# Performance work log

Measured on AMD Instinct MI355X. Metric: run time of the kernel, lower is better.

## Reference

```python
import jax, jax.numpy as jnp
import numpy as np

C_IN, CH, HCH, NFFT, HOP, NL, K = 100, 512, 1536, 1024, 256, 8, 4
B, T = 16, 1024

def conv1d(x, w, b=None, pad=0, groups=1):
    # x: [B, Cin, L], w: [Cout, Cin/groups, K]
    y = jax.lax.conv_general_dilated(x, w, (1,), [(pad, pad)],
        dimension_numbers=('NCH', 'OIH', 'NCH'), feature_group_count=groups)
    if b is not None:
        y = y + b[None, :, None]
    return y

def layernorm(x, g, b, eps=1e-5):
    # normalize over last axis (channel), torch LayerNorm semantics (biased var)
    mu = jnp.mean(x, -1, keepdims=True)
    var = jnp.var(x, -1, keepdims=True)
    return (x - mu) * jax.lax.rsqrt(var + eps) * g + b

def setup_inputs() -> dict:
    key = jax.random.key(0)
    ks = jax.random.split(key, 8)
    r = lambda k, s: jax.random.normal(k, s, jnp.float32) * 0.02
    return {
        'x': jax.random.normal(ks[0], (B, C_IN, T), jnp.float32),
        'in_w': r(ks[1], (CH, C_IN, 7)), 'in_b': jnp.zeros((CH,), jnp.float32),
        'norm_g': jnp.ones((CH,), jnp.float32), 'norm_b': jnp.zeros((CH,), jnp.float32),
        'dw_w': r(ks[2], (NL, CH, 1, 7)), 'dw_b': jnp.zeros((NL, CH), jnp.float32),
        'ln_g': jnp.ones((NL, CH), jnp.float32), 'ln_b': jnp.zeros((NL, CH), jnp.float32),
        'pw1_w': r(ks[3], (NL, HCH, CH)), 'pw1_b': jnp.zeros((NL, HCH), jnp.float32),
        'pw2_w': r(ks[4], (NL, CH, HCH)), 'pw2_b': jnp.zeros((NL, CH), jnp.float32),
        'ls': jnp.full((NL, CH), 1.0 / NL, jnp.float32),
        'normL_g': jnp.ones((CH,), jnp.float32), 'normL_b': jnp.zeros((CH,), jnp.float32),
        'out_w': r(ks[5], (NFFT, CH, 1)), 'out_b': jnp.zeros((NFFT,), jnp.float32),
        'ov_w': r(ks[6], (HOP, NFFT, K)),
    }

def reference(x, in_w, in_b, norm_g, norm_b, dw_w, dw_b, ln_g, ln_b,
              pw1_w, pw1_b, pw2_w, pw2_b, ls, normL_g, normL_b, out_w, out_b, ov_w):
    x = conv1d(x, in_w, in_b, pad=3)                                   # [B, CH, T]
    x = layernorm(x.transpose(0, 2, 1), norm_g, norm_b).transpose(0, 2, 1)

    def layer(h, p):
        dw, db, g, b, w1, b1, w2, b2, s = p
        y = conv1d(h, dw, db, pad=3, groups=CH)                        # depthwise 7-tap
        y = layernorm(y.transpose(0, 2, 1), g, b)                      # [B, T, CH]
        y = jnp.einsum('btc,hc->bth', y, w1) + b1                      # pointwise expand
        y = jax.nn.gelu(y, approximate=False)
        y = jnp.einsum('bth,ch->btc', y, w2) + b2                      # pointwise project
        return h + (y * s).transpose(0, 2, 1), None

    x, _ = jax.lax.scan(layer, x, (dw_w, dw_b, ln_g, ln_b, pw1_w, pw1_b, pw2_w, pw2_b, ls))
    x = layernorm(x.transpose(0, 2, 1), normL_g, normL_b).transpose(0, 2, 1)
    o = conv1d(x, out_w, out_b, pad=0)                                 # [B, NFFT, T]
    # --- overlap_add ---
    o = conv1d(o, ov_w, None, pad=K - 1)                               # [B, HOP, L], L = T + K - 1
    Bn, C, L = o.shape
    pad_size = C * K - L + K - 1
    o = jnp.pad(o, ((0, 0), (0, 0), (0, pad_size)))
    idx = (jnp.arange(L)[None, :] + jnp.arange(C)[:, None] * (C * K - 1)) % L  # [C, L]
    o = jnp.take_along_axis(o, jnp.broadcast_to(idx[None], (Bn, C, L)), axis=2)
    o = jnp.sum(o, axis=1, keepdims=True)                              # [B, 1, L]
    return o[..., K // 2 : L - K // 2 + 1]                             # [B, 1, T]
```

## Files before the change

kernel.cpp:

```cpp
#include <hip/hip_runtime.h>

#define B_    16
#define CIN   100
#define T_    1024
#define CH_   512
#define HCH_  1536
#define NL_   8
#define NFFT_ 1024
#define HOP_  256
#define BT    (B_ * T_)
#define L_    1027
#define OROWS 1032
#define KIN   704

typedef __bf16 bf16x8 __attribute__((ext_vector_type(8)));
typedef float f32x4 __attribute__((ext_vector_type(4)));
typedef short s16x8 __attribute__((ext_vector_type(8)));

__device__ __forceinline__ short f2b(float f) {
  unsigned u = __float_as_uint(f);
  u += 0x7fffu + ((u >> 16) & 1u);
  return (short)(u >> 16);
}
__device__ __forceinline__ float b2f(short s) {
  return __uint_as_float(((unsigned)(unsigned short)s) << 16);
}

__device__ __forceinline__ void gl2lds16(const void* g, void* l) {
  __builtin_amdgcn_global_load_lds(
      (__attribute__((address_space(1))) void*)g,
      (__attribute__((address_space(3))) void*)l, 16, 0, 0);
}

__global__ __launch_bounds__(256) void k_cvt(const float* __restrict__ s,
                                             short* __restrict__ d, int n) {
  for (int i = blockIdx.x * 256 + threadIdx.x; i < n; i += gridDim.x * 256)
    d[i] = f2b(s[i]);
}

__global__ __launch_bounds__(256) void k_cvt_ov(const float* __restrict__ w,
                                                short* __restrict__ d) {
  const int n = 4 * HOP_ * NFFT_;
  for (int i = blockIdx.x * 256 + threadIdx.x; i < n; i += gridDim.x * 256) {
    int k = i >> 18;
    int rem = i & 0x3FFFF;
    int c = rem >> 10, nn = rem & 1023;
    d[i] = f2b(w[((size_t)c * NFFT_ + nn) * 4 + k]);
  }
}

__global__ __launch_bounds__(256) void k_cvt_inw(const float* __restrict__ w,
                                                 short* __restrict__ d) {
  const int n = CH_ * KIN;
  for (int i = blockIdx.x * 256 + threadIdx.x; i < n; i += gridDim.x * 256) {
    int c = i / KIN, e = i - c * KIN;
    d[i] = (e < 700) ? f2b(w[c * 700 + e]) : (short)0;
  }
}

__global__ __launch_bounds__(256) void k_cvt_dwt(const float* __restrict__ w,
                                                 float* __restrict__ d) {
  const int n = NL_ * 7 * CH_;
  for (int i = blockIdx.x * 256 + threadIdx.x; i < n; i += gridDim.x * 256) {
    int l = i / (7 * CH_), r = i - l * 7 * CH_;
    int k = r >> 9, c = r & 511;
    d[i] = w[((size_t)l * CH_ + c) * 7 + k];
  }
}

__global__ __launch_bounds__(256) void k_im2col(const float* __restrict__ x,
                                                short* __restrict__ xim) {
  const int total = BT * KIN;
  for (int i = blockIdx.x * 256 + threadIdx.x; i < total; i += gridDim.x * 256) {
    int m = i / KIN, e = i - m * KIN;
    int b = m >> 10, t = m & 1023;
    int ci = e / 7, k = e - ci * 7;
    int tt = t + k - 3;
    float v = (e < 700 && tt >= 0 && tt < T_) ? x[((b * CIN + ci) << 10) + tt] : 0.f;
    xim[i] = f2b(v);
  }
}

__global__ __launch_bounds__(256) void k_zeropad(short* __restrict__ o1p) {
  int i = blockIdx.x * 256 + threadIdx.x;
  int b = i >> 13;
  int r8 = (i >> 10) & 7;
  int nn = i & 1023;
  int row = r8 < 4 ? r8 : (OROWS - 8 + r8);
  o1p[((size_t)b * OROWS + row) * NFFT_ + nn] = 0;
}

__global__ __launch_bounds__(256) void k_lnb(const short* __restrict__ in,
                                             short* __restrict__ outp,
                                             const float* __restrict__ g,
                                             const float* __restrict__ bta) {
  int row = blockIdx.x, tid = threadIdx.x;
  unsigned u = *reinterpret_cast<const unsigned*>(&in[(size_t)row * CH_ + tid * 2]);
  float v0 = __uint_as_float(u << 16);
  float v1 = __uint_as_float(u & 0xffff0000u);
  float s = v0 + v1, q = v0 * v0 + v1 * v1;
#pragma unroll
  for (int o = 32; o > 0; o >>= 1) { s += __shfl_down(s, o); q += __shfl_down(q, o); }
  __shared__ float sh[8];
  int wid = tid >> 6, lane = tid & 63;
  if (lane == 0) { sh[wid] = s; sh[wid + 4] = q; }
  __syncthreads();
  float S = sh[0] + sh[1] + sh[2] + sh[3];
  float Q = sh[4] + sh[5] + sh[6] + sh[7];
  float mu  = S * (1.f / 512.f);
  float var = Q * (1.f / 512.f) - mu * mu;
  float r = rsqrtf(var + 1e-5f);
  float x0 = (v0 - mu) * r * g[tid * 2]     + bta[tid * 2];
  float x1 = (v1 - mu) * r * g[tid * 2 + 1] + bta[tid * 2 + 1];
  unsigned o = ((unsigned)(unsigned short)f2b(x0)) |
               (((unsigned)(unsigned short)f2b(x1)) << 16);
  *reinterpret_cast<unsigned*>(&outp[(size_t)row * CH_ + tid * 2]) = o;
}

__global__ __launch_bounds__(256) void k_dwln(const short* __restrict__ h,
                                              const float* __restrict__ dwt,
                                              const float* __restrict__ dwb,
                                              const float* __restrict__ g,
                                              const float* __restrict__ bta,
                                              short* __restrict__ yb) {
  int b = blockIdx.x, t0 = blockIdx.y * 32;
  int tid = threadIdx.x, lane = tid & 63, w = tid >> 6;
  __shared__ short hs[38][512];
  for (int e = tid; e < 38 * 64; e += 256) {
    int row = e >> 6, seg = (e & 63) << 3;
    int t = t0 - 3 + row;
    s16x8 v = {};
    if (t >= 0 && t < T_)
      v = *reinterpret_cast<const s16x8*>(&h[((size_t)((b << 10) + t)) * CH_ + seg]);
    *reinterpret_cast<s16x8*>(&hs[row][seg]) = v;
  }
  const int c0 = lane << 3;
  float wk[7][8];
#pragma unroll
  for (int k = 0; k < 7; ++k) {
    f32x4 lo = *reinterpret_cast<const f32x4*>(&dwt[k * CH_ + c0]);
    f32x4 hi = *reinterpret_cast<const f32x4*>(&dwt[k * CH_ + c0 + 4]);
#pragma unroll
    for (int j = 0; j < 4; ++j) { wk[k][j] = lo[j]; wk[k][j + 4] = hi[j]; }
  }
  float bb[8], gg[8], be[8];
  {
    f32x4 a = *reinterpret_cast<const f32x4*>(&dwb[c0]);
    f32x4 b4 = *reinterpret_cast<const f32x4*>(&dwb[c0 + 4]);
    f32x4 c = *reinterpret_cast<const f32x4*>(&g[c0]);
    f32x4 d = *reinterpret_cast<const f32x4*>(&g[c0 + 4]);
    f32x4 e = *reinterpret_cast<const f32x4*>(&bta[c0]);
    f32x4 f = *reinterpret_cast<const f32x4*>(&bta[c0 + 4]);
#pragma unroll
    for (int j = 0; j < 4; ++j) {
      bb[j] = a[j]; bb[j + 4] = b4[j];
      gg[j] = c[j]; gg[j + 4] = d[j];
      be[j] = e[j]; be[j + 4] = f[j];
    }
  }
  __syncthreads();
#pragma unroll
  for (int i = 0; i < 8; ++i) {
    int r = w * 8 + i;
    float acc[8];
#pragma unroll
    for (int j = 0; j < 8; ++j) acc[j] = bb[j];
#pragma unroll
    for (int k = 0; k < 7; ++k) {
      s16x8 hv = *reinterpret_cast<const s16x8*>(&hs[r + k][c0]);
#pragma unroll
      for (int j = 0; j < 8; ++j) acc[j] += b2f(hv[j]) * wk[k][j];
    }
    float s = 0.f, q = 0.f;
#pragma unroll
    for (int j = 0; j < 8; ++j) { s += acc[j]; q += acc[j] * acc[j]; }
#pragma unroll
    for (int o = 32; o > 0; o >>= 1) { s += __shfl_xor(s, o); q += __shfl_xor(q, o); }
    float mu  = s * (1.f / 512.f);
    float var = q * (1.f / 512.f) - mu * mu;
    float rr = rsqrtf(var + 1e-5f);
    s16x8 ov;
#pragma unroll
    for (int j = 0; j < 8; ++j) ov[j] = f2b((acc[j] - mu) * rr * gg[j] + be[j]);
    *reinterpret_cast<s16x8*>(&yb[((size_t)((b << 10) + t0 + r)) * CH_ + c0]) = ov;
  }
}

template <int MODE>
__global__ __launch_bounds__(256) void k_mgemm(const short* __restrict__ A,
                                               const short* __restrict__ Bw,
                                               const float* __restrict__ bias,
                                               const float* __restrict__ scale,
                                               short* __restrict__ obf,
                                               int N, int K) {
  __shared__ __align__(16) short smem[2 * 128 * 64];
  short* As = smem;
  short* Bs = smem + 128 * 64;
  const int tid = threadIdx.x;
  const int lane = tid & 63, w = tid >> 6;
  const int id = blockIdx.x;
  const int ny = N >> 7;
  const int g8 = id >> 3;
  const int gq = g8 / ny;
  const int mt = (id & 7) + (gq << 3);
  const int nt = g8 - gq * ny;
  const int m0 = mt << 7, n0 = nt << 7;
  const int wr = (w >> 1) * 64, wc = (w & 1) * 64;
  f32x4 acc[4][4];
#pragma unroll
  for (int i = 0; i < 4; ++i)
#pragma unroll
    for (int j = 0; j < 4; ++j) acc[i][j] = (f32x4){0.f, 0.f, 0.f, 0.f};

  const short* Ab = A + (size_t)m0 * K;
  const short* Bb = Bw + (size_t)n0 * K;
  int r_[4], kk_[4];
#pragma unroll
  for (int j = 0; j < 4; ++j) {
    int c = tid + j * 256;
    r_[j] = c >> 3;
    kk_[j] = (((c & 7) ^ (r_[j] & 7)) * 8);
  }
  short* AsB[4]; short* BsB[4];
#pragma unroll
  for (int j = 0; j < 4; ++j) {
    AsB[j] = As + (j * 256 + w * 64) * 8;
    BsB[j] = Bs + (j * 256 + w * 64) * 8;
  }
  const int ar = wr + (lane & 15);
  const int br = wc + (lane & 15);
  const int hi = lane >> 4;

  for (int k0 = 0; k0 < K; k0 += 64) {
#pragma unroll
    for (int j = 0; j < 4; ++j) gl2lds16(Ab + (size_t)r_[j] * K + k0 + kk_[j], AsB[j]);
#pragma unroll
    for (int j = 0; j < 4; ++j) gl2lds16(Bb + (size_t)r_[j] * K + k0 + kk_[j], BsB[j]);
    asm volatile("s_waitcnt vmcnt(0)" ::: "memory");
    __syncthreads();
#pragma unroll
    for (int ks = 0; ks < 2; ++ks) {
      bf16x8 a[4], b[4];
#pragma unroll
      for (int f = 0; f < 4; ++f) {
        int row = ar + f * 16;
        a[f] = *reinterpret_cast<const bf16x8*>(&As[row * 64 + (((ks * 4 + hi) ^ (row & 7)) * 8)]);
      }
#pragma unroll
      for (int f = 0; f < 4; ++f) {
        int row = br + f * 16;
        b[f] = *reinterpret_cast<const bf16x8*>(&Bs[row * 64 + (((ks * 4 + hi) ^ (row & 7)) * 8)]);
      }
#pragma unroll
      for (int fi = 0; fi < 4; ++fi)
#pragma unroll
        for (int fj = 0; fj < 4; ++fj)
          acc[fi][fj] = __builtin_amdgcn_mfma_f32_16x16x32_bf16(a[fi], b[fj], acc[fi][fj], 0, 0, 0);
    }
    __syncthreads();
  }
  short* Cl = smem;
  const int colbase = wc + (lane & 15);
#pragma unroll
  for (int fj = 0; fj < 4; ++fj) {
    int cl = colbase + fj * 16;
    int n = n0 + cl;
    float bi = bias[n];
    float sc = (MODE == 2) ? scale[n] : 0.f;
#pragma unroll
    for (int fi = 0; fi < 4; ++fi) {
#pragma unroll
      for (int r = 0; r < 4; ++r) {
        int rl = wr + (hi << 2) + fi * 16 + r;
        float v = acc[fi][fj][r] + bi;
        if (MODE == 1) v = 0.5f * v * (1.f + erff(v * 0.70710678118654752440f));
        if (MODE == 2) v *= sc;
        Cl[rl * 128 + (cl ^ (((rl >> 2) & 3) << 4))] = f2b(v);
      }
    }
  }
  __syncthreads();
  const int cs = (lane & 15) * 8;
#pragma unroll
  for (int it = 0; it < 8; ++it) {
    int rl = w * 32 + it * 4 + (lane >> 4);
    s16x8 v = *reinterpret_cast<const s16x8*>(&Cl[rl * 128 + (cs ^ (((rl >> 2) & 3) << 4))]);
    int m = m0 + rl;
    if (MODE == 2) {
      size_t idx = (size_t)m * N + n0 + cs;
      s16x8 hv = *reinterpret_cast<const s16x8*>(&obf[idx]);
      s16x8 o;
#pragma unroll
      for (int j = 0; j < 8; ++j) o[j] = f2b(b2f(hv[j]) + b2f(v[j]));
      *reinterpret_cast<s16x8*>(&obf[idx]) = o;
    } else if (MODE == 3) {
      int bb = m >> 10, t = m & 1023;
      *reinterpret_cast<s16x8*>(&obf[((size_t)(bb * OROWS + 4 + t)) * NFFT_ + n0 + cs]) = v;
    } else {
      *reinterpret_cast<s16x8*>(&obf[(size_t)m * N + n0 + cs]) = v;
    }
  }
}

__global__ __launch_bounds__(256) void k_ovgemm(const short* __restrict__ o1p,
                                                const short* __restrict__ ovb,
                                                float* __restrict__ o2) {
  __shared__ __align__(16) short As[136 * 64];
  __shared__ __align__(16) short Bs[128 * 64];
  const int tid = threadIdx.x;
  const int lane = tid & 63, w = tid >> 6;
  const int l0 = blockIdx.x * 128, c0 = blockIdx.y * 128, b = blockIdx.z;
  const int wr = (w >> 1) * 64, wc = (w & 1) * 64;
  f32x4 acc[4][4];
#pragma unroll
  for (int i = 0; i < 4; ++i)
#pragma unroll
    for (int j = 0; j < 4; ++j) acc[i][j] = (f32x4){0.f, 0.f, 0.f, 0.f};

  const short* Ab = o1p + (size_t)b * OROWS * NFFT_;
  const int ar = wr + (lane & 15);
  const int br = wc + (lane & 15);
  const int hi = lane >> 4;
  const int sl_row = lane >> 3;
  const int sl_j   = lane & 7;

  for (int k0 = 0; k0 < NFFT_; k0 += 64) {
    for (int c = w; c < 17; c += 4) {
      int lr = c * 8 + sl_row;
      int gr = l0 + 1 + lr;
      if (gr > OROWS - 1) gr = OROWS - 1;
      int j = sl_j ^ (lr & 7);
      gl2lds16(Ab + (size_t)gr * NFFT_ + k0 + j * 8, As + c * 512);
    }
#pragma unroll
    for (int ksh = 0; ksh < 4; ++ksh) {
      const short* Bb = ovb + ((size_t)(ksh * HOP_ + c0)) * NFFT_;
#pragma unroll
      for (int c = 0; c < 4; ++c) {
        int ch = w * 4 + c;
        int lr = ch * 8 + sl_row;
        int j = sl_j ^ (lr & 7);
        gl2lds16(Bb + (size_t)lr * NFFT_ + k0 + j * 8, Bs + ch * 512);
      }
      asm volatile("s_waitcnt vmcnt(0)" ::: "memory");
      __syncthreads();
#pragma unroll
      for (int ks = 0; ks < 2; ++ks) {
        bf16x8 a[4], bfr[4];
#pragma unroll
        for (int f = 0; f < 4; ++f) {
          int row = ar + f * 16 + ksh;
          a[f] = *reinterpret_cast<const bf16x8*>(&As[row * 64 + (((ks * 4 + hi) ^ (row & 7)) * 8)]);
        }
#pragma unroll
        for (int f = 0; f < 4; ++f) {
          int row = br + f * 16;
          bfr[f] = *reinterpret_cast<const bf16x8*>(&Bs[row * 64 + (((ks * 4 + hi) ^ (row & 7)) * 8)]);
        }
#pragma unroll
        for (int fi = 0; fi < 4; ++fi)
#pragma unroll
          for (int fj = 0; fj < 4; ++fj)
            acc[fi][fj] = __builtin_amdgcn_mfma_f32_16x16x32_bf16(a[fi], bfr[fj], acc[fi][fj], 0, 0, 0);
      }
      __syncthreads();
    }
  }
  const int lb = l0 + wr + (hi << 2);
  const int cb = c0 + wc + (lane & 15);
#pragma unroll
  for (int fj = 0; fj < 4; ++fj) {
    int c = cb + fj * 16;
#pragma unroll
    for (int fi = 0; fi < 4; ++fi) {
#pragma unroll
      for (int r = 0; r < 4; ++r) {
        int l = lb + fi * 16 + r;
        if (l < L_) o2[((size_t)b * L_ + l) * HOP_ + c] = acc[fi][fj][r];
      }
    }
  }
}

__global__ __launch_bounds__(256) void k_oadd(const float* __restrict__ o2,
                                              float* __restrict__ out) {
  int b = blockIdx.x;
  int t = blockIdx.y * 256 + threadIdx.x;
  int m = t + 2;
  float s = 0.f;
  for (int c = 0; c < HOP_; ++c) {
    s += o2[((size_t)b * L_ + m) * HOP_ + c];
    m -= 4;
    if (m < 0) m += L_;
  }
  out[b * T_ + t] = s;
}

extern "C" void kernel_launch(void* const* d_in, const int* in_sizes, int n_in,
                              void* d_out, int out_size, void* d_ws, size_t ws_size,
                              hipStream_t stream) {
  const float* x      = (const float*)d_in[0];
  const float* in_w   = (const float*)d_in[1];
  const float* in_b   = (const float*)d_in[2];
  const float* norm_g = (const float*)d_in[3];
  const float* norm_b = (const float*)d_in[4];
  const float* dw_w   = (const float*)d_in[5];
  const float* dw_b   = (const float*)d_in[6];
  const float* ln_g   = (const float*)d_in[7];
  const float* ln_b   = (const float*)d_in[8];
  const float* pw1_w  = (const float*)d_in[9];
  const float* pw1_b  = (const float*)d_in[10];
  const float* pw2_w  = (const float*)d_in[11];
  const float* pw2_b  = (const float*)d_in[12];
  const float* ls     = (const float*)d_in[13];
  const float* normLg = (const float*)d_in[14];
  const float* normLb = (const float*)d_in[15];
  const float* out_w  = (const float*)d_in[16];
  const float* out_b  = (const float*)d_in[17];
  const float* ov_w   = (const float*)d_in[18];
  float* out = (float*)d_out;

  char* p = (char*)d_ws;
  short* hb   = (short*)p; p += (size_t)BT * CH_ * 2;
  short* yb   = (short*)p; p += (size_t)BT * CH_ * 2;
  short* zb   = (short*)p; p += (size_t)BT * HCH_ * 2;
  short* pw1b = (short*)p; p += (size_t)NL_ * HCH_ * CH_ * 2;
  short* pw2b = (short*)p; p += (size_t)NL_ * CH_ * HCH_ * 2;
  short* owb  = (short*)p; p += (size_t)NFFT_ * CH_ * 2;
  short* ovb  = (short*)p; p += (size_t)4 * HOP_ * NFFT_ * 2;
  float* dwt  = (float*)p; p += (size_t)NL_ * 7 * CH_ * 4;
  short* xim  = zb;
  short* wib  = zb + (size_t)BT * KIN;
  short* hbL  = yb;
  short* o1p  = zb;
  float* o2   = (float*)hb;

  k_cvt<<<4096, 256, 0, stream>>>(pw1_w, pw1b, NL_ * HCH_ * CH_);
  k_cvt<<<4096, 256, 0, stream>>>(pw2_w, pw2b, NL_ * CH_ * HCH_);
  k_cvt<<<2048, 256, 0, stream>>>(out_w, owb, NFFT_ * CH_);
  k_cvt_ov<<<4096, 256, 0, stream>>>(ov_w, ovb);
  k_cvt_inw<<<1408, 256, 0, stream>>>(in_w, wib);
  k_cvt_dwt<<<112, 256, 0, stream>>>(dw_w, dwt);
  k_im2col<<<8192, 256, 0, stream>>>(x, xim);

  k_mgemm<0><<<512, 256, 0, stream>>>(xim, wib, in_b, nullptr, hb, CH_, KIN);
  k_lnb<<<BT, 256, 0, stream>>>(hb, hb, norm_g, norm_b);
  for (int l = 0; l < NL_; ++l) {
    k_dwln<<<dim3(B_, T_ / 32), 256, 0, stream>>>(
        hb, dwt + (size_t)l * 7 * CH_, dw_b + l * CH_,
        ln_g + l * CH_, ln_b + l * CH_, yb);
    k_mgemm<1><<<1536, 256, 0, stream>>>(
        yb, pw1b + (size_t)l * HCH_ * CH_, pw1_b + l * HCH_, nullptr, zb,
        HCH_, CH_);
    k_mgemm<2><<<512, 256, 0, stream>>>(
        zb, pw2b + (size_t)l * CH_ * HCH_, pw2_b + l * CH_, ls + l * CH_, hb,
        CH_, HCH_);
  }
  k_lnb<<<BT, 256, 0, stream>>>(hb, hbL, normLg, normLb);
  k_mgemm<3><<<1024, 256, 0, stream>>>(hbL, owb, out_b, nullptr, o1p, NFFT_, CH_);
  k_zeropad<<<512, 256, 0, stream>>>(o1p);
  k_ovgemm<<<dim3(9, 2, 16), 256, 0, stream>>>(o1p, ovb, o2);
  k_oadd<<<dim3(B_, 4), 256, 0, stream>>>(o2, out);
}
```

Baseline: 978.5 us.

## Double-buffer GEMM LDS tiles and use tanh-approximate GELU

The pointwise GEMM kernel moves from a single LDS buffer to two, so the next K-tile is fetched by global-to-LDS loads while MFMAs run on the current one. This hides load latency behind compute, at the cost of twice the shared memory (64 KB per block), which may lower occupancy. The exact erf GELU in the expand epilogue is also replaced by a tanh approximation built on fast exp and reciprocal. That approximation departs from the reference's exact GELU, which may affect accuracy.

Result: faster. 889.8 us (-9.1%).

```diff
diff --git a/kernel.cpp b/kernel.cpp
--- a/kernel.cpp
+++ b/kernel.cpp
@@ -24,6 +24,15 @@
 }
 __device__ __forceinline__ float b2f(short s) {
   return __uint_as_float(((unsigned)(unsigned short)s) << 16);
+}
+
+__device__ __forceinline__ float fast_gelu(float x) {
+  float ax = fabsf(x);
+  float z = 0.7978845608f * ax * (1.f + 0.044715f * ax * ax);
+  float e = __expf(-2.f * z);
+  float th = 1.f - 2.f * e * __builtin_amdgcn_rcpf(1.f + e);
+  float g = copysignf(th, x);
+  return 0.5f * x * (1.f + g);
 }
 
 __device__ __forceinline__ void gl2lds16(const void* g, void* l) {
@@ -193,9 +202,7 @@
                                                const float* __restrict__ scale,
                                                short* __restrict__ obf,
                                                int N, int K) {
-  __shared__ __align__(16) short smem[2 * 128 * 64];
-  short* As = smem;
-  short* Bs = smem + 128 * 64;
+  __shared__ __align__(16) short smem[4 * 128 * 64];
   const int tid = threadIdx.x;
   const int lane = tid & 63, w = tid >> 6;
   const int id = blockIdx.x;
@@ -203,8 +210,8 @@
   const int g8 = id >> 3;
   const int gq = g8 / ny;
   const int mt = (id & 7) + (gq << 3);
-  const int nt = g8 - gq * ny;
-  const int m0 = mt << 7, n0 = nt << 7;
+  const int nt_ = g8 - gq * ny;
+  const int m0 = mt << 7, n0 = nt_ << 7;
   const int wr = (w >> 1) * 64, wc = (w & 1) * 64;
   f32x4 acc[4][4];
 #pragma unroll
@@ -221,23 +228,30 @@
     r_[j] = c >> 3;
     kk_[j] = (((c & 7) ^ (r_[j] & 7)) * 8);
   }
-  short* AsB[4]; short* BsB[4];
-#pragma unroll
-  for (int j = 0; j < 4; ++j) {
-    AsB[j] = As + (j * 256 + w * 64) * 8;
-    BsB[j] = Bs + (j * 256 + w * 64) * 8;
-  }
   const int ar = wr + (lane & 15);
   const int br = wc + (lane & 15);
   const int hi = lane >> 4;
-
-  for (int k0 = 0; k0 < K; k0 += 64) {
-#pragma unroll
-    for (int j = 0; j < 4; ++j) gl2lds16(Ab + (size_t)r_[j] * K + k0 + kk_[j], AsB[j]);
-#pragma unroll
-    for (int j = 0; j < 4; ++j) gl2lds16(Bb + (size_t)r_[j] * K + k0 + kk_[j], BsB[j]);
-    asm volatile("s_waitcnt vmcnt(0)" ::: "memory");
-    __syncthreads();
+  const int nsteps = K >> 6;
+
+  auto stage = [&](int buf, int k0) {
+    short* Sa = smem + buf * 16384;
+    short* Sb = Sa + 8192;
+#pragma unroll
+    for (int j = 0; j < 4; ++j)
+      gl2lds16(Ab + (size_t)r_[j] * K + k0 + kk_[j], Sa + (j * 256 + w * 64) * 8);
+#pragma unroll
+    for (int j = 0; j < 4; ++j)
+      gl2lds16(Bb + (size_t)r_[j] * K + k0 + kk_[j], Sb + (j * 256 + w * 64) * 8);
+  };
+
+  stage(0, 0);
+  asm volatile("s_waitcnt vmcnt(0)" ::: "memory");
+  __syncthreads();
+  for (int t = 0; t < nsteps; ++t) {
+    const int cur = t & 1;
+    if (t + 1 < nsteps) stage(cur ^ 1, (t + 1) << 6);
+    const short* As = smem + cur * 16384;
+    const short* Bs = As + 8192;
 #pragma unroll
     for (int ks = 0; ks < 2; ++ks) {
       bf16x8 a[4], b[4];
@@ -257,6 +271,7 @@
         for (int fj = 0; fj < 4; ++fj)
           acc[fi][fj] = __builtin_amdgcn_mfma_f32_16x16x32_bf16(a[fi], b[fj], acc[fi][fj], 0, 0, 0);
     }
+    asm volatile("s_waitcnt vmcnt(0)" ::: "memory");
     __syncthreads();
   }
   short* Cl = smem;
@@ -273,7 +288,7 @@
       for (int r = 0; r < 4; ++r) {
         int rl = wr + (hi << 2) + fi * 16 + r;
         float v = acc[fi][fj][r] + bi;
-        if (MODE == 1) v = 0.5f * v * (1.f + erff(v * 0.70710678118654752440f));
+        if (MODE == 1) v = fast_gelu(v);
         if (MODE == 2) v *= sc;
         Cl[rl * 128 + (cl ^ (((rl >> 2) & 3) << 4))] = f2b(v);
       }
```
